# Performance work log

Measured on AMD Instinct MI355X. Metric: run time of the kernel, lower is better.

Reference implementation:

```python
import jax, jax.numpy as jnp
import numpy as np

SIGMA = 5.0  # Gaussian kernel bandwidth
GAMMA = 1.0 / (2.0 * SIGMA * SIGMA)


def setup_inputs() -> dict:
    key = jax.random.key(0)
    k1, k2, k3 = jax.random.split(key, 3)
    x = jax.random.normal(k1, (8192, 128), dtype=jnp.float32)
    centers = jax.random.normal(k2, (50000, 128), dtype=jnp.float32)
    weight = jax.random.normal(k3, (50000, 10), dtype=jnp.float32) * 0.05
    return {"x": x, "centers": centers, "weight": weight}


def _gaussian_kernel(x, centers):
    x2 = jnp.sum(x * x, axis=1, keepdims=True)            # [n_x, 1]
    c2 = jnp.sum(centers * centers, axis=1)               # [n_centers]
    d2 = x2 + c2[None, :] - 2.0 * (x @ centers.T)
    d2 = jnp.maximum(d2, 0.0)
    return jnp.exp(-GAMMA * d2)


def reference(x, centers, weight):
    # forward: K = kernel(x, centers); p = K @ weight
    K = _gaussian_kernel(x, centers)                      # [8192, 50000]
    return K @ weight                                     # [8192, 10]
```

## Files before the change

kernel.cpp:

```cpp
#include <hip/hip_runtime.h>
#include <hip/hip_fp8.h>


#define NX 8192
#define NC 50000
#define DD 128
#define NO 10
#define BN 64
#define NTILES 782
#define NCHUNK 24
#define MBLKS 32
#define GRID_MAIN (MBLKS * NCHUNK)

#define GAMMA 0.02f
#define LOG2E 1.4426950408889634f
#define GLOG2E (GAMMA * LOG2E)
#define S2G (2.0f * GAMMA * LOG2E)
#define XSCALE (S2G * 16.0f)
#define SCALE_ONE 0x7F7F7F7Fu
#define SCALE_B16 0x7B7B7B7Bu

#define OFF_XIMG 0ull
#define OFF_XSC  1048576ull
#define OFF_CIMG 1081344ull
#define OFF_WIMG 7487488ull
#define WS_NEED  10690560ull

typedef __attribute__((ext_vector_type(8))) short short8;
typedef __attribute__((ext_vector_type(4))) float f32x4;
typedef __attribute__((ext_vector_type(16))) float f32x16;
typedef __attribute__((ext_vector_type(4))) int i32x4;
typedef __attribute__((ext_vector_type(8))) int i32x8;

__device__ __forceinline__ unsigned pk_bf16(float a, float b) {
  union { float f; unsigned u; } ua, ub;
  ua.f = a; ub.f = b;
  unsigned ha = (ua.u + 0x7FFFu + ((ua.u >> 16) & 1u)) >> 16;
  unsigned hb = (ub.u + 0x7FFFu + ((ub.u >> 16) & 1u)) >> 16;
  return (hb << 16) | (ha & 0xFFFFu);
}
__device__ __forceinline__ unsigned short bf16_1(float a) {
  union { float f; unsigned u; } ua;
  ua.f = a;
  return (unsigned short)((ua.u + 0x7FFFu + ((ua.u >> 16) & 1u)) >> 16);
}
__device__ __forceinline__ unsigned char to_fp8(float v) {
  return (unsigned char)__hip_cvt_float_to_fp8(v, __HIP_SATFINITE, __HIP_E4M3);
}
__device__ __forceinline__ uint4 fp8x16(const float* v, float s) {
  unsigned w[4];
#pragma unroll
  for (int i = 0; i < 4; ++i) {
    w[i] = (unsigned)to_fp8(s * v[4 * i + 0]) |
           ((unsigned)to_fp8(s * v[4 * i + 1]) << 8) |
           ((unsigned)to_fp8(s * v[4 * i + 2]) << 16) |
           ((unsigned)to_fp8(s * v[4 * i + 3]) << 24);
  }
  return make_uint4(w[0], w[1], w[2], w[3]);
}


__global__ void pre_all(const float* __restrict__ x, const float* __restrict__ cent,
                        const float* __restrict__ w, char* __restrict__ ws) {
  const int b = blockIdx.x, t = threadIdx.x;
  if (b < 64) {
    char* img = ws + OFF_XIMG + (size_t)b * 16384;
#pragma unroll
    for (int i = 0; i < 4; ++i) {
      int q = i * 256 + t;
      int g_local = q >> 8;
      int r = q & 255;
      int fid = r >> 6;
      int lane = r & 63;
      int ks2 = fid >> 1, half = fid & 1;
      int m = b * 128 + g_local * 32 + (lane & 31);
      int k0 = ks2 * 64 + (lane >> 5) * 32 + half * 16;
      float v[16];
      *(float4*)&v[0] = *(const float4*)(x + (size_t)m * DD + k0);
      *(float4*)&v[4] = *(const float4*)(x + (size_t)m * DD + k0 + 4);
      *(float4*)&v[8] = *(const float4*)(x + (size_t)m * DD + k0 + 8);
      *(float4*)&v[12] = *(const float4*)(x + (size_t)m * DD + k0 + 12);
      *(uint4*)(img + g_local * 4096 + fid * 1024 + lane * 16) = fp8x16(v, XSCALE);
    }
    if (t < 128) {
      const int m = b * 128 + t;
      const float4* r4 = (const float4*)(x + (size_t)m * DD);
      float s = 0.f;
#pragma unroll
      for (int k = 0; k < 32; ++k) {
        float4 v = r4[k];
        s += v.x * v.x + v.y * v.y + v.z * v.z + v.w * v.w;
      }
      ((float*)(ws + OFF_XSC))[m] = __builtin_amdgcn_exp2f(-GLOG2E * s);
    }
  } else {
    const int tile = b - 64;
    __shared__ float sNF[BN];
    {
      const int c_loc = t >> 2;
      const int part = t & 3;
      const int c = tile * BN + c_loc;
      float s = 0.f;
      if (c < NC) {
        const float4* r4 = (const float4*)(cent + (size_t)c * DD) + part * 8;
#pragma unroll
        for (int k = 0; k < 8; ++k) {
          float4 v = r4[k];
          s += v.x * v.x + v.y * v.y + v.z * v.z + v.w * v.w;
        }
      }
      s += __shfl_xor(s, 1);
      s += __shfl_xor(s, 2);
      if (part == 0) sNF[c_loc] = __builtin_amdgcn_exp2f(-GLOG2E * s);
    }
    __syncthreads();

    {
      char* img = ws + OFF_CIMG + (size_t)tile * 8192;
#pragma unroll
      for (int i = 0; i < 2; ++i) {
        int q = i * 256 + t;
        int fid = q >> 6;
        int lane = q & 63;
        int ct = fid >> 2, ks2 = (fid >> 1) & 1, half = fid & 1;
        int c = tile * BN + ct * 32 + (lane & 31);
        int k0 = ks2 * 64 + (lane >> 5) * 32 + half * 16;
        float v[16];
        if (c < NC) {
          *(float4*)&v[0] = *(const float4*)(cent + (size_t)c * DD + k0);
          *(float4*)&v[4] = *(const float4*)(cent + (size_t)c * DD + k0 + 4);
          *(float4*)&v[8] = *(const float4*)(cent + (size_t)c * DD + k0 + 8);
          *(float4*)&v[12] = *(const float4*)(cent + (size_t)c * DD + k0 + 12);
        } else {
#pragma unroll
          for (int j = 0; j < 16; ++j) v[j] = 0.f;
        }
        *(uint4*)(img + fid * 1024 + lane * 16) = fp8x16(v, 1.0f);
      }
    }

    {
      const int l = t & 63, gg = t >> 6;
      const int j = l & 31, hi = l >> 5;
      const int clbase = gg * 16 + hi * 8;
      unsigned d[4];
#pragma unroll
      for (int i = 0; i < 4; ++i) {
        int cl0 = clbase + 2 * i;
        int c0 = tile * BN + cl0;
        float w0 = 0.f, w1 = 0.f;
        if (j < NO) {
          if (c0 < NC) w0 = w[(size_t)c0 * NO + j] * sNF[cl0];
          if (c0 + 1 < NC) w1 = w[(size_t)(c0 + 1) * NO + j] * sNF[cl0 + 1];
        }
        d[i] = pk_bf16(w0, w1);
      }
      *(uint4*)(ws + OFF_WIMG + (size_t)tile * 4096 + t * 16) =
          make_uint4(d[0], d[1], d[2], d[3]);
    }
  }
}


__device__ __forceinline__ void gld16(const char* g, const char* l) {
  __builtin_amdgcn_global_load_lds(
      (const __attribute__((address_space(1))) unsigned int*)g,
      (__attribute__((address_space(3))) unsigned int*)l, 16, 0, 0);
}

__device__ __forceinline__ short8 gload16(const char* p) {
  short8 r;
  asm volatile("global_load_dwordx4 %0, %1, off" : "=v"(r) : "v"(p));
  return r;
}
__device__ __forceinline__ i32x4 gload16i(const char* p) {
  i32x4 r;
  asm volatile("global_load_dwordx4 %0, %1, off" : "=v"(r) : "v"(p));
  return r;
}

__device__ __forceinline__ unsigned cvtpk(float lo, float hi2) {
  unsigned r;
  asm volatile("v_cvt_pk_bf16_f32 %0, %1, %2" : "=v"(r) : "v"(lo), "v"(hi2));
  return r;
}
__device__ __forceinline__ void swap32(unsigned& a, unsigned& b) {
  asm volatile("v_permlane32_swap_b32 %0, %1" : "+v"(a), "+v"(b));
}
__device__ __forceinline__ short8 mk8(unsigned a, unsigned b, unsigned c, unsigned d) {
  union { unsigned u[4]; short8 s; } z;
  z.u[0] = a; z.u[1] = b; z.u[2] = c; z.u[3] = d;
  return z.s;
}
__device__ __forceinline__ i32x8 cat8(i32x4 lo, i32x4 hi) {
  union { i32x4 h[2]; i32x8 w; } z;
  z.h[0] = lo; z.h[1] = hi;
  return z.w;
}

__device__ __forceinline__ void pack32(const f32x16 acc, short8& pE, short8& pO) {
  float p[16];
#pragma unroll
  for (int r = 0; r < 16; ++r) p[r] = __builtin_amdgcn_exp2f(acc[r]);
  unsigned a0 = cvtpk(p[0], p[1]);
  unsigned a1 = cvtpk(p[2], p[3]);
  unsigned a2 = cvtpk(p[4], p[5]);
  unsigned a3 = cvtpk(p[6], p[7]);
  unsigned b0 = cvtpk(p[8], p[9]);
  unsigned b1 = cvtpk(p[10], p[11]);
  unsigned b2 = cvtpk(p[12], p[13]);
  unsigned b3 = cvtpk(p[14], p[15]);
  swap32(a0, a2);
  swap32(a1, a3);
  swap32(b0, b2);
  swap32(b1, b3);
  pE = mk8(a0, a1, a2, a3);
  pO = mk8(b0, b1, b2, b3);
}

__global__ void __launch_bounds__(256, 3) eigenpro_mfma(
    const char* __restrict__ ws, float* __restrict__ out) {
  __shared__ int4 sB[3][512];

  const int t = threadIdx.x;
  const int lane = t & 63;
  const int wid = t >> 6;
  const int l31 = lane & 31;
  const int hi = lane >> 5;

  const int chunk = blockIdx.x % NCHUNK;
  const int mb = blockIdx.x / NCHUNK;

  const char* cimg = ws + OFF_CIMG;
  const char* wimg = ws + OFF_WIMG;
  const float* xs = (const float*)(ws + OFF_XSC);

  const int t0 = chunk * 32 + (chunk < 14 ? chunk : 14);
  const int nt = 32 + (chunk < 14 ? 1 : 0);

  i32x8 xf[2][2];
#pragma unroll
  for (int mf = 0; mf < 2; ++mf) {
    const char* xg =
        ws + OFF_XIMG + (size_t)(mb * 8 + wid * 2 + mf) * 4096 + lane * 16;
    i32x4 h[4];
#pragma unroll
    for (int fh = 0; fh < 4; ++fh) h[fh] = gload16i(xg + fh * 1024);
    xf[mf][0] = cat8(h[0], h[1]);
    xf[mf][1] = cat8(h[2], h[3]);
  }
  __builtin_amdgcn_sched_barrier(0);
  {
    const char* cg = cimg + (size_t)t0 * 8192 + wid * 1024 + lane * 16;
    const char* cl = (const char*)&sB[0][0] + wid * 1024;
    gld16(cg, cl);
    gld16(cg + 4096, cl + 4096);
  }
  asm volatile("s_waitcnt vmcnt(2)" ::: "memory");
  __builtin_amdgcn_sched_barrier(0);

  const f32x16 zero16 = {0.f, 0.f, 0.f, 0.f, 0.f, 0.f, 0.f, 0.f,
                         0.f, 0.f, 0.f, 0.f, 0.f, 0.f, 0.f, 0.f};
  f32x16 pv0 = zero16, pv1 = zero16;

  int cur = 0;
#pragma unroll 1
  for (int it = 0; it < nt; ++it) {
    const int nxt = (cur == 2) ? 0 : cur + 1;
    const char* Bt = (const char*)&sB[cur][0];

    const char* wg = wimg + (size_t)(t0 + it) * 4096 + lane * 16;
    short8 wfr[4];
    wfr[0] = gload16(wg);
    wfr[1] = gload16(wg + 1024);
    wfr[2] = gload16(wg + 2048);
    wfr[3] = gload16(wg + 3072);
    __builtin_amdgcn_sched_barrier(0);

    const int has_next = (it + 1 < nt);
    if (has_next) {
      const char* cg = cimg + (size_t)(t0 + it + 1) * 8192 + wid * 1024 + lane * 16;
      const char* cl = (const char*)&sB[nxt][0] + wid * 1024;
      gld16(cg, cl);
      gld16(cg + 4096, cl + 4096);
      asm volatile("s_waitcnt vmcnt(6)" ::: "memory");
    } else {
      asm volatile("s_waitcnt vmcnt(4)" ::: "memory");
    }
    __builtin_amdgcn_s_barrier();
    __builtin_amdgcn_sched_barrier(0);

#pragma unroll
    for (int ct = 0; ct < 2; ++ct) {
      f32x16 acc0 = zero16, acc1 = zero16;
#pragma unroll
      for (int ks2 = 0; ks2 < 2; ++ks2) {
        const char* fb = Bt + ((ct * 2 + ks2) * 2) * 1024 + lane * 16;
        i32x4 lo = *(const i32x4*)fb;
        i32x4 hi4 = *(const i32x4*)(fb + 1024);
        i32x8 ca = cat8(lo, hi4);
        acc0 = __builtin_amdgcn_mfma_scale_f32_32x32x64_f8f6f4(
            ca, xf[0][ks2], acc0, 0, 0, 0, SCALE_ONE, 0, SCALE_B16);
        acc1 = __builtin_amdgcn_mfma_scale_f32_32x32x64_f8f6f4(
            ca, xf[1][ks2], acc1, 0, 0, 0, SCALE_ONE, 0, SCALE_B16);
      }

      short8 paE0, paO0, paE1, paO1;
      pack32(acc0, paE0, paO0);
      pack32(acc1, paE1, paO1);

      if (ct == 0) {
        if (has_next) {
          asm volatile("s_waitcnt vmcnt(2)" ::: "memory");
        } else {
          asm volatile("s_waitcnt vmcnt(0)" ::: "memory");
        }
        __builtin_amdgcn_sched_barrier(0);
      }
      pv0 = __builtin_amdgcn_mfma_f32_32x32x16_bf16(paE0, wfr[2 * ct], pv0, 0, 0, 0);
      pv1 = __builtin_amdgcn_mfma_f32_32x32x16_bf16(paE1, wfr[2 * ct], pv1, 0, 0, 0);
      pv0 = __builtin_amdgcn_mfma_f32_32x32x16_bf16(paO0, wfr[2 * ct + 1], pv0, 0, 0, 0);
      pv1 = __builtin_amdgcn_mfma_f32_32x32x16_bf16(paO1, wfr[2 * ct + 1], pv1, 0, 0, 0);
    }
    cur = nxt;
  }

  if (l31 < NO) {
#pragma unroll
    for (int r = 0; r < 16; ++r) {
      int mloc = (r & 3) + 8 * (r >> 2) + 4 * hi;
      int m0 = mb * 256 + wid * 64 + mloc;
      atomicAdd(&out[(size_t)m0 * NO + l31], pv0[r] * xs[m0]);
      atomicAdd(&out[(size_t)(m0 + 32) * NO + l31], pv1[r] * xs[m0 + 32]);
    }
  }
}


__global__ void eigenpro_sqnorm(const float* __restrict__ x,
                                const float* __restrict__ cent,
                                float* __restrict__ ws) {
  int i = blockIdx.x * blockDim.x + threadIdx.x;
  if (i >= NX + NC) return;
  const float* row = (i < NX) ? (x + (size_t)i * DD) : (cent + (size_t)(i - NX) * DD);
  const float4* r4 = (const float4*)row;
  float s = 0.f;
#pragma unroll
  for (int k = 0; k < DD / 4; ++k) {
    float4 v = r4[k];
    s += v.x * v.x + v.y * v.y + v.z * v.z + v.w * v.w;
  }
  ws[i] = -GLOG2E * s;
}

__device__ __forceinline__ void stage_tile8(const float* __restrict__ src, int nrows,
                                            short* dst, int t) {
  int col4 = t & 31;
  int rb = t >> 5;
#pragma unroll
  for (int i = 0; i < 16; ++i) {
    int row = rb + 8 * i;
    float4 v = make_float4(0.f, 0.f, 0.f, 0.f);
    if (row < nrows) v = *(const float4*)(src + (size_t)row * DD + col4 * 4);
    unsigned lo = pk_bf16(v.x, v.y), hi = pk_bf16(v.z, v.w);
    char* p = (char*)dst + row * 256 + ((col4 * 8) ^ ((row & 7) << 4));
    *(uint2*)p = make_uint2(lo, hi);
  }
}

__device__ __forceinline__ short8 ld_frag8(const short* base, int row, int kbyte) {
  const char* p = (const char*)base + row * 256 + (kbyte ^ ((row & 7) << 4));
  return *(const short8*)p;
}

__global__ void __launch_bounds__(256, 2) eigenpro_main_fb(
    const float* __restrict__ x, const float* __restrict__ cent,
    const float* __restrict__ w, const float* __restrict__ ws2,
    float* __restrict__ out) {
  __shared__ short sA[128 * DD];
  __shared__ short sBP[128 * DD];
  __shared__ short sWt[16 * 128];
  __shared__ float sC2[128];

  const int t = threadIdx.x;
  const int lane = t & 63;
  const int wid = t >> 6;
  const int l15 = lane & 15;
  const int g = lane >> 4;

  const int chunk = blockIdx.x & 7;
  const int mb = blockIdx.x >> 3;
  const int m0 = mb * 128;
  const int wrow0 = wid * 32;

  const float* ws_x2 = ws2;
  const float* ws_c2 = ws2 + NX;

  stage_tile8(x + (size_t)m0 * DD, 128, sA, t);

  float u[2][4];
#pragma unroll
  for (int mf = 0; mf < 2; ++mf)
#pragma unroll
    for (int r = 0; r < 4; ++r)
      u[mf][r] = ws_x2[m0 + wrow0 + mf * 16 + 4 * g + r];

  const f32x4 zero4 = {0.f, 0.f, 0.f, 0.f};
  f32x4 pv[2];
  pv[0] = zero4;
  pv[1] = zero4;

  const int nt128 = 391;
  const int tp = 49;
  const int t0 = chunk * tp;
  const int t1 = (t0 + tp < nt128) ? (t0 + tp) : nt128;

  for (int tile = t0; tile < t1; ++tile) {
    const int c0 = tile * 128;
    int nrows = NC - c0; if (nrows > 128) nrows = 128;

    __syncthreads();
    stage_tile8(cent + (size_t)c0 * DD, nrows, sBP, t);
    if (t < 128) {
      int c = c0 + t;
      sC2[t] = (c < NC) ? ws_c2[c] : -3.0e38f;
      float wrow[NO];
#pragma unroll
      for (int j = 0; j < NO; ++j) wrow[j] = (c < NC) ? w[(size_t)c * NO + j] : 0.f;
#pragma unroll
      for (int j = 0; j < 16; ++j) {
        unsigned short h = (j < NO && c < NC) ? bf16_1(wrow[j]) : (unsigned short)0;
        *(short*)((char*)sWt + j * 256 + ((2 * t) ^ ((j & 7) << 4))) = (short)h;
      }
    }
    __syncthreads();

    float v[8];
#pragma unroll
    for (int nf = 0; nf < 8; ++nf) v[nf] = sC2[nf * 16 + l15];

    short8 a[2][4];
#pragma unroll
    for (int mf = 0; mf < 2; ++mf)
#pragma unroll
      for (int ks = 0; ks < 4; ++ks)
        a[mf][ks] = ld_frag8(sA, wrow0 + mf * 16 + l15, ks * 64 + g * 16);

    f32x4 acc[2][8];
#pragma unroll
    for (int mf = 0; mf < 2; ++mf)
#pragma unroll
      for (int nf = 0; nf < 8; ++nf) acc[mf][nf] = zero4;

#pragma unroll
    for (int nf = 0; nf < 8; ++nf) {
#pragma unroll
      for (int ks = 0; ks < 4; ++ks) {
        short8 b = ld_frag8(sBP, nf * 16 + l15, ks * 64 + g * 16);
        acc[0][nf] = __builtin_amdgcn_mfma_f32_16x16x32_bf16(a[0][ks], b, acc[0][nf], 0, 0, 0);
        acc[1][nf] = __builtin_amdgcn_mfma_f32_16x16x32_bf16(a[1][ks], b, acc[1][nf], 0, 0, 0);
      }
    }

    __syncthreads();

#pragma unroll
    for (int mf = 0; mf < 2; ++mf) {
#pragma unroll
      for (int nf = 0; nf < 8; ++nf) {
#pragma unroll
        for (int r = 0; r < 4; ++r) {
          float s = acc[mf][nf][r];
          float arg = fmaf(s, 2.f * GAMMA * LOG2E, u[mf][r] + v[nf]);
          arg = fminf(arg, 0.f);
          float p = __builtin_amdgcn_exp2f(arg);
          int mrow = wrow0 + mf * 16 + 4 * g + r;
          *(short*)((char*)sBP + mrow * 256 + ((2 * (nf * 16 + l15)) ^ ((mrow & 7) << 4))) =
              (short)bf16_1(p);
        }
      }
    }
    __syncthreads();

#pragma unroll
    for (int ks = 0; ks < 4; ++ks) {
      short8 bw = ld_frag8(sWt, l15, ks * 64 + g * 16);
#pragma unroll
      for (int mf = 0; mf < 2; ++mf) {
        short8 pa = ld_frag8(sBP, wrow0 + mf * 16 + l15, ks * 64 + g * 16);
        pv[mf] = __builtin_amdgcn_mfma_f32_16x16x32_bf16(pa, bw, pv[mf], 0, 0, 0);
      }
    }
  }

  if (l15 < NO) {
#pragma unroll
    for (int mf = 0; mf < 2; ++mf) {
#pragma unroll
      for (int r = 0; r < 4; ++r) {
        int m = m0 + wrow0 + mf * 16 + 4 * g + r;
        atomicAdd(&out[(size_t)m * NO + l15], pv[mf][r]);
      }
    }
  }
}


extern "C" void kernel_launch(void* const* d_in, const int* in_sizes, int n_in,
                              void* d_out, int out_size, void* d_ws, size_t ws_size,
                              hipStream_t stream) {
  const float* x = (const float*)d_in[0];
  const float* cent = (const float*)d_in[1];
  const float* w = (const float*)d_in[2];
  float* out = (float*)d_out;

  hipMemsetAsync(d_out, 0, (size_t)out_size * sizeof(float), stream);

  if (ws_size >= WS_NEED) {
    pre_all<<<64 + NTILES, 256, 0, stream>>>(x, cent, w, (char*)d_ws);
    eigenpro_mfma<<<GRID_MAIN, 256, 0, stream>>>((const char*)d_ws, out);
  } else {
    float* ws = (float*)d_ws;
    int nrows = NX + NC;
    eigenpro_sqnorm<<<(nrows + 255) / 256, 256, 0, stream>>>(x, cent, ws);
    eigenpro_main_fb<<<64 * 8, 256, 0, stream>>>(x, cent, w, ws, out);
  }
}
```

Baseline: 98.67 us.

## Software-pipeline second GEMM one stage behind the distance MFMAs

Restructures the inner loop so the bf16 projection MFMAs for the previous column sub-tile run while the fp8 distance MFMAs for the current sub-tile are issued, carrying packed exp results and weight fragments in registers across stages. This is meant to hide the dependency latency between the distance accumulation, the exp/pack step and the weight MFMA. A drain step after the loop flushes the last stage. The cost is more live registers, which may reduce occupancy, plus some extra zero-valued MFMAs on the first iteration.

```diff
diff --git a/kernel.cpp b/kernel.cpp
--- a/kernel.cpp
+++ b/kernel.cpp
@@ -173,11 +173,6 @@
   asm volatile("global_load_dwordx4 %0, %1, off" : "=v"(r) : "v"(p));
   return r;
 }
-__device__ __forceinline__ i32x4 gload16i(const char* p) {
-  i32x4 r;
-  asm volatile("global_load_dwordx4 %0, %1, off" : "=v"(r) : "v"(p));
-  return r;
-}
 
 __device__ __forceinline__ unsigned cvtpk(float lo, float hi2) {
   unsigned r;
@@ -245,7 +240,11 @@
         ws + OFF_XIMG + (size_t)(mb * 8 + wid * 2 + mf) * 4096 + lane * 16;
     i32x4 h[4];
 #pragma unroll
-    for (int fh = 0; fh < 4; ++fh) h[fh] = gload16i(xg + fh * 1024);
+    for (int fh = 0; fh < 4; ++fh) {
+      i32x4 r;
+      asm volatile("global_load_dwordx4 %0, %1, off" : "=v"(r) : "v"(xg + fh * 1024));
+      h[fh] = r;
+    }
     xf[mf][0] = cat8(h[0], h[1]);
     xf[mf][1] = cat8(h[2], h[3]);
   }
@@ -261,7 +260,11 @@
 
   const f32x16 zero16 = {0.f, 0.f, 0.f, 0.f, 0.f, 0.f, 0.f, 0.f,
                          0.f, 0.f, 0.f, 0.f, 0.f, 0.f, 0.f, 0.f};
+  const short8 zero8 = {0, 0, 0, 0, 0, 0, 0, 0};
   f32x16 pv0 = zero16, pv1 = zero16;
+
+  short8 paS0 = zero8, paS1 = zero8, paS2 = zero8, paS3 = zero8;
+  short8 wS0 = zero8, wS1 = zero8;
 
   int cur = 0;
 #pragma unroll 1
@@ -270,11 +273,10 @@
     const char* Bt = (const char*)&sB[cur][0];
 
     const char* wg = wimg + (size_t)(t0 + it) * 4096 + lane * 16;
-    short8 wfr[4];
-    wfr[0] = gload16(wg);
-    wfr[1] = gload16(wg + 1024);
-    wfr[2] = gload16(wg + 2048);
-    wfr[3] = gload16(wg + 3072);
+    short8 wfr0 = gload16(wg);
+    short8 wfr1 = gload16(wg + 1024);
+    short8 wfr2 = gload16(wg + 2048);
+    short8 wfr3 = gload16(wg + 3072);
     __builtin_amdgcn_sched_barrier(0);
 
     const int has_next = (it + 1 < nt);
@@ -290,40 +292,64 @@
     __builtin_amdgcn_s_barrier();
     __builtin_amdgcn_sched_barrier(0);
 
-#pragma unroll
-    for (int ct = 0; ct < 2; ++ct) {
+    {
       f32x16 acc0 = zero16, acc1 = zero16;
 #pragma unroll
       for (int ks2 = 0; ks2 < 2; ++ks2) {
-        const char* fb = Bt + ((ct * 2 + ks2) * 2) * 1024 + lane * 16;
-        i32x4 lo = *(const i32x4*)fb;
-        i32x4 hi4 = *(const i32x4*)(fb + 1024);
-        i32x8 ca = cat8(lo, hi4);
+        const char* fb = Bt + (ks2 * 2) * 1024 + lane * 16;
+        i32x8 ca = cat8(*(const i32x4*)fb, *(const i32x4*)(fb + 1024));
         acc0 = __builtin_amdgcn_mfma_scale_f32_32x32x64_f8f6f4(
             ca, xf[0][ks2], acc0, 0, 0, 0, SCALE_ONE, 0, SCALE_B16);
         acc1 = __builtin_amdgcn_mfma_scale_f32_32x32x64_f8f6f4(
             ca, xf[1][ks2], acc1, 0, 0, 0, SCALE_ONE, 0, SCALE_B16);
       }
-
-      short8 paE0, paO0, paE1, paO1;
-      pack32(acc0, paE0, paO0);
-      pack32(acc1, paE1, paO1);
-
-      if (ct == 0) {
-        if (has_next) {
-          asm volatile("s_waitcnt vmcnt(2)" ::: "memory");
-        } else {
-          asm volatile("s_waitcnt vmcnt(0)" ::: "memory");
-        }
-        __builtin_amdgcn_sched_barrier(0);
-      }
-      pv0 = __builtin_amdgcn_mfma_f32_32x32x16_bf16(paE0, wfr[2 * ct], pv0, 0, 0, 0);
-      pv1 = __builtin_amdgcn_mfma_f32_32x32x16_bf16(paE1, wfr[2 * ct], pv1, 0, 0, 0);
-      pv0 = __builtin_amdgcn_mfma_f32_32x32x16_bf16(paO0, wfr[2 * ct + 1], pv0, 0, 0, 0);
-      pv1 = __builtin_amdgcn_mfma_f32_32x32x16_bf16(paO1, wfr[2 * ct + 1], pv1, 0, 0, 0);
-    }
+      pv0 = __builtin_amdgcn_mfma_f32_32x32x16_bf16(paS0, wS0, pv0, 0, 0, 0);
+      pv1 = __builtin_amdgcn_mfma_f32_32x32x16_bf16(paS2, wS0, pv1, 0, 0, 0);
+      pv0 = __builtin_amdgcn_mfma_f32_32x32x16_bf16(paS1, wS1, pv0, 0, 0, 0);
+      pv1 = __builtin_amdgcn_mfma_f32_32x32x16_bf16(paS3, wS1, pv1, 0, 0, 0);
+
+      if (has_next) {
+        asm volatile("s_waitcnt vmcnt(2)" ::: "memory");
+      } else {
+        asm volatile("s_waitcnt vmcnt(0)" ::: "memory");
+      }
+      __builtin_amdgcn_sched_barrier(0);
+
+      pack32(acc0, paS0, paS1);
+      pack32(acc1, paS2, paS3);
+      wS0 = wfr0;
+      wS1 = wfr1;
+    }
+
+    {
+      f32x16 acc0 = zero16, acc1 = zero16;
+#pragma unroll
+      for (int ks2 = 0; ks2 < 2; ++ks2) {
+        const char* fb = Bt + ((2 + ks2) * 2) * 1024 + lane * 16;
+        i32x8 ca = cat8(*(const i32x4*)fb, *(const i32x4*)(fb + 1024));
+        acc0 = __builtin_amdgcn_mfma_scale_f32_32x32x64_f8f6f4(
+            ca, xf[0][ks2], acc0, 0, 0, 0, SCALE_ONE, 0, SCALE_B16);
+        acc1 = __builtin_amdgcn_mfma_scale_f32_32x32x64_f8f6f4(
+            ca, xf[1][ks2], acc1, 0, 0, 0, SCALE_ONE, 0, SCALE_B16);
+      }
+      pv0 = __builtin_amdgcn_mfma_f32_32x32x16_bf16(paS0, wS0, pv0, 0, 0, 0);
+      pv1 = __builtin_amdgcn_mfma_f32_32x32x16_bf16(paS2, wS0, pv1, 0, 0, 0);
+      pv0 = __builtin_amdgcn_mfma_f32_32x32x16_bf16(paS1, wS1, pv0, 0, 0, 0);
+      pv1 = __builtin_amdgcn_mfma_f32_32x32x16_bf16(paS3, wS1, pv1, 0, 0, 0);
+
+      pack32(acc0, paS0, paS1);
+      pack32(acc1, paS2, paS3);
+      wS0 = wfr2;
+      wS1 = wfr3;
+    }
+
     cur = nxt;
   }
+
+  pv0 = __builtin_amdgcn_mfma_f32_32x32x16_bf16(paS0, wS0, pv0, 0, 0, 0);
+  pv1 = __builtin_amdgcn_mfma_f32_32x32x16_bf16(paS2, wS0, pv1, 0, 0, 0);
+  pv0 = __builtin_amdgcn_mfma_f32_32x32x16_bf16(paS1, wS1, pv0, 0, 0, 0);
+  pv1 = __builtin_amdgcn_mfma_f32_32x32x16_bf16(paS3, wS1, pv1, 0, 0, 0);
 
   if (l31 < NO) {
 #pragma unroll
```

After: 100.3 us. No clear change (+1.7%).

## Replace LDS triple-buffered center staging with direct register prefetch of fragments

Applied to the files above, without the earlier changes.

Removes the shared-memory ring buffer, the async global-to-LDS loads and the per-iteration workgroup barrier. Each wave now loads its center and weight fragments straight from global memory into registers, one half-tile ahead, using a software double buffer. The inline-asm loads and hand-placed waitcnt/sched barriers are dropped and scheduling is left to the compiler. The cost is that every wave fetches the full center tile itself instead of sharing one LDS copy, which raises global/L2 traffic and register pressure.

```diff
diff --git a/kernel.cpp b/kernel.cpp
--- a/kernel.cpp
+++ b/kernel.cpp
@@ -162,23 +162,6 @@
 }
 
 
-__device__ __forceinline__ void gld16(const char* g, const char* l) {
-  __builtin_amdgcn_global_load_lds(
-      (const __attribute__((address_space(1))) unsigned int*)g,
-      (__attribute__((address_space(3))) unsigned int*)l, 16, 0, 0);
-}
-
-__device__ __forceinline__ short8 gload16(const char* p) {
-  short8 r;
-  asm volatile("global_load_dwordx4 %0, %1, off" : "=v"(r) : "v"(p));
-  return r;
-}
-__device__ __forceinline__ i32x4 gload16i(const char* p) {
-  i32x4 r;
-  asm volatile("global_load_dwordx4 %0, %1, off" : "=v"(r) : "v"(p));
-  return r;
-}
-
 __device__ __forceinline__ unsigned cvtpk(float lo, float hi2) {
   unsigned r;
   asm volatile("v_cvt_pk_bf16_f32 %0, %1, %2" : "=v"(r) : "v"(lo), "v"(hi2));
@@ -220,8 +203,6 @@
 
 __global__ void __launch_bounds__(256, 3) eigenpro_mfma(
     const char* __restrict__ ws, float* __restrict__ out) {
-  __shared__ int4 sB[3][512];
-
   const int t = threadIdx.x;
   const int lane = t & 63;
   const int wid = t >> 6;
@@ -237,92 +218,78 @@
 
   const int t0 = chunk * 32 + (chunk < 14 ? chunk : 14);
   const int nt = 32 + (chunk < 14 ? 1 : 0);
+  const int nq = nt * 2;
 
   i32x8 xf[2][2];
 #pragma unroll
   for (int mf = 0; mf < 2; ++mf) {
     const char* xg =
         ws + OFF_XIMG + (size_t)(mb * 8 + wid * 2 + mf) * 4096 + lane * 16;
-    i32x4 h[4];
-#pragma unroll
-    for (int fh = 0; fh < 4; ++fh) h[fh] = gload16i(xg + fh * 1024);
-    xf[mf][0] = cat8(h[0], h[1]);
-    xf[mf][1] = cat8(h[2], h[3]);
-  }
-  __builtin_amdgcn_sched_barrier(0);
-  {
-    const char* cg = cimg + (size_t)t0 * 8192 + wid * 1024 + lane * 16;
-    const char* cl = (const char*)&sB[0][0] + wid * 1024;
-    gld16(cg, cl);
-    gld16(cg + 4096, cl + 4096);
-  }
-  asm volatile("s_waitcnt vmcnt(2)" ::: "memory");
-  __builtin_amdgcn_sched_barrier(0);
+    i32x4 h0 = *(const i32x4*)(xg);
+    i32x4 h1 = *(const i32x4*)(xg + 1024);
+    i32x4 h2 = *(const i32x4*)(xg + 2048);
+    i32x4 h3 = *(const i32x4*)(xg + 3072);
+    xf[mf][0] = cat8(h0, h1);
+    xf[mf][1] = cat8(h2, h3);
+  }
 
   const f32x16 zero16 = {0.f, 0.f, 0.f, 0.f, 0.f, 0.f, 0.f, 0.f,
                          0.f, 0.f, 0.f, 0.f, 0.f, 0.f, 0.f, 0.f};
   f32x16 pv0 = zero16, pv1 = zero16;
 
-  int cur = 0;
+  i32x4 cfA0, cfA1, cfA2, cfA3;
+  short8 wfA0, wfA1;
+  {
+    const char* cb = cimg + (size_t)t0 * 8192 + lane * 16;
+    cfA0 = *(const i32x4*)cb;
+    cfA1 = *(const i32x4*)(cb + 1024);
+    cfA2 = *(const i32x4*)(cb + 2048);
+    cfA3 = *(const i32x4*)(cb + 3072);
+    const char* wb = wimg + (size_t)t0 * 4096 + lane * 16;
+    wfA0 = *(const short8*)wb;
+    wfA1 = *(const short8*)(wb + 1024);
+  }
+
 #pragma unroll 1
-  for (int it = 0; it < nt; ++it) {
-    const int nxt = (cur == 2) ? 0 : cur + 1;
-    const char* Bt = (const char*)&sB[cur][0];
-
-    const char* wg = wimg + (size_t)(t0 + it) * 4096 + lane * 16;
-    short8 wfr[4];
-    wfr[0] = gload16(wg);
-    wfr[1] = gload16(wg + 1024);
-    wfr[2] = gload16(wg + 2048);
-    wfr[3] = gload16(wg + 3072);
-    __builtin_amdgcn_sched_barrier(0);
-
-    const int has_next = (it + 1 < nt);
-    if (has_next) {
-      const char* cg = cimg + (size_t)(t0 + it + 1) * 8192 + wid * 1024 + lane * 16;
-      const char* cl = (const char*)&sB[nxt][0] + wid * 1024;
-      gld16(cg, cl);
-      gld16(cg + 4096, cl + 4096);
-      asm volatile("s_waitcnt vmcnt(6)" ::: "memory");
-    } else {
-      asm volatile("s_waitcnt vmcnt(4)" ::: "memory");
-    }
-    __builtin_amdgcn_s_barrier();
-    __builtin_amdgcn_sched_barrier(0);
-
-#pragma unroll
-    for (int ct = 0; ct < 2; ++ct) {
-      f32x16 acc0 = zero16, acc1 = zero16;
-#pragma unroll
-      for (int ks2 = 0; ks2 < 2; ++ks2) {
-        const char* fb = Bt + ((ct * 2 + ks2) * 2) * 1024 + lane * 16;
-        i32x4 lo = *(const i32x4*)fb;
-        i32x4 hi4 = *(const i32x4*)(fb + 1024);
-        i32x8 ca = cat8(lo, hi4);
-        acc0 = __builtin_amdgcn_mfma_scale_f32_32x32x64_f8f6f4(
-            ca, xf[0][ks2], acc0, 0, 0, 0, SCALE_ONE, 0, SCALE_B16);
-        acc1 = __builtin_amdgcn_mfma_scale_f32_32x32x64_f8f6f4(
-            ca, xf[1][ks2], acc1, 0, 0, 0, SCALE_ONE, 0, SCALE_B16);
-      }
-
-      short8 paE0, paO0, paE1, paO1;
-      pack32(acc0, paE0, paO0);
-      pack32(acc1, paE1, paO1);
-
-      if (ct == 0) {
-        if (has_next) {
-          asm volatile("s_waitcnt vmcnt(2)" ::: "memory");
-        } else {
-          asm volatile("s_waitcnt vmcnt(0)" ::: "memory");
-        }
-        __builtin_amdgcn_sched_barrier(0);
-      }
-      pv0 = __builtin_amdgcn_mfma_f32_32x32x16_bf16(paE0, wfr[2 * ct], pv0, 0, 0, 0);
-      pv1 = __builtin_amdgcn_mfma_f32_32x32x16_bf16(paE1, wfr[2 * ct], pv1, 0, 0, 0);
-      pv0 = __builtin_amdgcn_mfma_f32_32x32x16_bf16(paO0, wfr[2 * ct + 1], pv0, 0, 0, 0);
-      pv1 = __builtin_amdgcn_mfma_f32_32x32x16_bf16(paO1, wfr[2 * ct + 1], pv1, 0, 0, 0);
-    }
-    cur = nxt;
+  for (int q = 0; q < nq; ++q) {
+    i32x4 cfB0, cfB1, cfB2, cfB3;
+    short8 wfB0, wfB1;
+    {
+      int qq = (q + 1 < nq) ? (q + 1) : q;
+      const char* cb =
+          cimg + (size_t)(t0 + (qq >> 1)) * 8192 + (qq & 1) * 4096 + lane * 16;
+      cfB0 = *(const i32x4*)cb;
+      cfB1 = *(const i32x4*)(cb + 1024);
+      cfB2 = *(const i32x4*)(cb + 2048);
+      cfB3 = *(const i32x4*)(cb + 3072);
+      const char* wb =
+          wimg + (size_t)(t0 + (qq >> 1)) * 4096 + (qq & 1) * 2048 + lane * 16;
+      wfB0 = *(const short8*)wb;
+      wfB1 = *(const short8*)(wb + 1024);
+    }
+
+    i32x8 ca0 = cat8(cfA0, cfA1);
+    i32x8 ca1 = cat8(cfA2, cfA3);
+    f32x16 acc0 = __builtin_amdgcn_mfma_scale_f32_32x32x64_f8f6f4(
+        ca0, xf[0][0], zero16, 0, 0, 0, SCALE_ONE, 0, SCALE_B16);
+    acc0 = __builtin_amdgcn_mfma_scale_f32_32x32x64_f8f6f4(
+        ca1, xf[0][1], acc0, 0, 0, 0, SCALE_ONE, 0, SCALE_B16);
+    f32x16 acc1 = __builtin_amdgcn_mfma_scale_f32_32x32x64_f8f6f4(
+        ca0, xf[1][0], zero16, 0, 0, 0, SCALE_ONE, 0, SCALE_B16);
+    acc1 = __builtin_amdgcn_mfma_scale_f32_32x32x64_f8f6f4(
+        ca1, xf[1][1], acc1, 0, 0, 0, SCALE_ONE, 0, SCALE_B16);
+
+    short8 paE0, paO0, paE1, paO1;
+    pack32(acc0, paE0, paO0);
+    pack32(acc1, paE1, paO1);
+
+    pv0 = __builtin_amdgcn_mfma_f32_32x32x16_bf16(paE0, wfA0, pv0, 0, 0, 0);
+    pv1 = __builtin_amdgcn_mfma_f32_32x32x16_bf16(paE1, wfA0, pv1, 0, 0, 0);
+    pv0 = __builtin_amdgcn_mfma_f32_32x32x16_bf16(paO0, wfA1, pv0, 0, 0, 0);
+    pv1 = __builtin_amdgcn_mfma_f32_32x32x16_bf16(paO1, wfA1, pv1, 0, 0, 0);
+
+    cfA0 = cfB0; cfA1 = cfB1; cfA2 = cfB2; cfA3 = cfB3;
+    wfA0 = wfB0; wfA1 = wfB1;
   }
 
   if (l31 < NO) {
```

Measured after the change: 99.56 us. Within noise of the previous version (+0.9%).
